# Performance work log

Measured on AMD Instinct MI355X. Metric: run time of the kernel, lower is better.

## Reference

```python
import jax, jax.numpy as jnp
import numpy as np

N_NODES = 200000
N_EDGES = 12800000
N_FEAT = 256


def setup_inputs() -> dict:
    key = jax.random.key(0)
    k1, k2, k3, k4 = jax.random.split(key, 4)
    x = jax.random.normal(k1, (N_NODES, N_FEAT), dtype=jnp.float32)
    edge_index = jax.random.randint(k2, (2, N_EDGES), 0, N_NODES, dtype=jnp.int64)
    attrs = jax.random.uniform(k3, (N_EDGES,), dtype=jnp.float32)
    W = jax.random.normal(k4, (N_FEAT, 1), dtype=jnp.float32) * (1.0 / np.sqrt(N_FEAT))
    b = jnp.zeros((1,), dtype=jnp.float32)
    return {"x": x, "edge_index": edge_index, "attrs": attrs, "W": W, "b": b}


def reference(x, edge_index, attrs, W, b):
    # GCNConv(num_features, 1) with edge_weight=attrs, default add_self_loops=True, normalize=True
    N = x.shape[0]
    row, col = edge_index[0], edge_index[1]  # source, target
    loop = jnp.arange(N, dtype=edge_index.dtype)
    row = jnp.concatenate([row, loop])
    col = jnp.concatenate([col, loop])
    w = jnp.concatenate([attrs, jnp.ones((N,), dtype=x.dtype)])
    # symmetric normalization: deg over targets with edge weights
    deg = jax.ops.segment_sum(w, col, num_segments=N)
    dis = jnp.where(deg > 0, jax.lax.rsqrt(deg), jnp.zeros_like(deg))
    norm = dis[row] * w * dis[col]  # [E+N]
    h = x @ W  # [N, 1]
    msg = norm[:, None] * h[row]  # gather + weight, [E+N, 1]
    out = jax.ops.segment_sum(msg, col, num_segments=N) + b  # scatter-add, [N, 1]
    out = out * jnp.tanh(jax.nn.softplus(out))  # Mish
    return out.reshape(1, -1)
```

## Files before the change

### kernel.cpp

```cpp
#include <hip/hip_runtime.h>
#include <hip/hip_fp16.h>
#include <math.h>
#include <stdint.h>


#define NFEAT 256
#define SPAN 4096
#define SPAN_BITS 12
#define MAXBKT 64
#define SEG 16
#define BCAP 266240
#define TILE 6144
#define PBT 512
#define BBT 512

__global__ void k_zero_u32(unsigned* __restrict__ p, int n) {
    int i = blockIdx.x * blockDim.x + threadIdx.x;
    if (i < n) p[i] = 0u;
}

__global__ void k_matvec(const float* __restrict__ x,
                         const float* __restrict__ W,
                         float* __restrict__ h, int N) {
    int gid  = blockIdx.x * blockDim.x + threadIdx.x;
    int node = gid >> 6;
    int lane = gid & 63;
    if (node >= N) return;
    float4 xv = ((const float4*)(x + (size_t)node * NFEAT))[lane];
    float4 wv = ((const float4*)W)[lane];
    float s = xv.x * wv.x + xv.y * wv.y + xv.z * wv.z + xv.w * wv.w;
#pragma unroll
    for (int off = 32; off > 0; off >>= 1)
        s += __shfl_down(s, off, 64);
    if (lane == 0) h[node] = s;
}

__global__ void __launch_bounds__(PBT) k_partition(
        const int* __restrict__ row, const int* __restrict__ col,
        const float* __restrict__ attrs,
        unsigned* __restrict__ g_cnt,
        unsigned* __restrict__ keys, __half* __restrict__ att16,
        int E, int nbkt) {
    __shared__ unsigned lhist[MAXBKT];
    __shared__ unsigned lstart[MAXBKT];
    __shared__ unsigned lcur[MAXBKT];
    __shared__ unsigned lbase[MAXBKT];
    __shared__ unsigned lkey[TILE];
    __shared__ unsigned short latt[TILE];

    const int tid = threadIdx.x;
    const int e0  = blockIdx.x * TILE;
    const int e1  = min(e0 + TILE, E);
    const int nv  = (e1 - e0) & ~3;

    if (tid < MAXBKT) lhist[tid] = 0u;
    __syncthreads();
    for (int o = tid << 2; o < nv; o += PBT << 2) {
        int4 c4 = *(const int4*)(col + e0 + o);
        atomicAdd(&lhist[((unsigned)c4.x) >> SPAN_BITS], 1u);
        atomicAdd(&lhist[((unsigned)c4.y) >> SPAN_BITS], 1u);
        atomicAdd(&lhist[((unsigned)c4.z) >> SPAN_BITS], 1u);
        atomicAdd(&lhist[((unsigned)c4.w) >> SPAN_BITS], 1u);
    }
    for (int e = e0 + nv + tid; e < e1; e += PBT)
        atomicAdd(&lhist[((unsigned)col[e]) >> SPAN_BITS], 1u);
    __syncthreads();
    if (tid == 0) {
        unsigned s = 0;
        for (int b = 0; b < nbkt; ++b) { lstart[b] = s; s += lhist[b]; }
    }
    if (tid < nbkt) lbase[tid] = atomicAdd(&g_cnt[tid], lhist[tid]);
    __syncthreads();
    if (tid < nbkt) lcur[tid] = lstart[tid];
    __syncthreads();

    for (int o = tid << 2; o < nv; o += PBT << 2) {
        const int e = e0 + o;
        int4   c4 = *(const int4*)(col + e);
        int4   r4 = *(const int4*)(row + e);
        float4 a4 = *(const float4*)(attrs + e);
        {
            unsigned c = (unsigned)c4.x, bkt = c >> SPAN_BITS;
            unsigned t = atomicAdd(&lcur[bkt], 1u);
            lkey[t] = ((unsigned)r4.x << SPAN_BITS) | (c & (SPAN - 1));
            latt[t] = __half_as_ushort(__float2half(a4.x));
        }
        {
            unsigned c = (unsigned)c4.y, bkt = c >> SPAN_BITS;
            unsigned t = atomicAdd(&lcur[bkt], 1u);
            lkey[t] = ((unsigned)r4.y << SPAN_BITS) | (c & (SPAN - 1));
            latt[t] = __half_as_ushort(__float2half(a4.y));
        }
        {
            unsigned c = (unsigned)c4.z, bkt = c >> SPAN_BITS;
            unsigned t = atomicAdd(&lcur[bkt], 1u);
            lkey[t] = ((unsigned)r4.z << SPAN_BITS) | (c & (SPAN - 1));
            latt[t] = __half_as_ushort(__float2half(a4.z));
        }
        {
            unsigned c = (unsigned)c4.w, bkt = c >> SPAN_BITS;
            unsigned t = atomicAdd(&lcur[bkt], 1u);
            lkey[t] = ((unsigned)r4.w << SPAN_BITS) | (c & (SPAN - 1));
            latt[t] = __half_as_ushort(__float2half(a4.w));
        }
    }
    for (int e = e0 + nv + tid; e < e1; e += PBT) {
        unsigned c   = (unsigned)col[e];
        unsigned bkt = c >> SPAN_BITS;
        unsigned t   = atomicAdd(&lcur[bkt], 1u);
        lkey[t] = ((unsigned)row[e] << SPAN_BITS) | (c & (SPAN - 1));
        latt[t] = __half_as_ushort(__float2half(attrs[e]));
    }
    __syncthreads();

    const int wave = tid >> 6, lane = tid & 63;
    for (int b = wave; b < nbkt; b += (PBT / 64)) {
        const unsigned cnt = lhist[b];
        const unsigned gb  = lbase[b];
        const unsigned ls  = lstart[b];
        const size_t base  = (size_t)b * BCAP;
        for (unsigned i = lane; i < cnt; i += 64) {
            unsigned t = gb + i;
            if (t < BCAP) {
                keys[base + t]  = lkey[ls + i];
                att16[base + t] = __ushort_as_half(latt[ls + i]);
            }
        }
    }
}

__global__ void __launch_bounds__(BBT) k_bucket_deg(
        const unsigned* __restrict__ g_cnt, const unsigned* __restrict__ keys,
        const __half* __restrict__ att16, float* __restrict__ rep, int npad) {
    __shared__ float acc[SPAN];
    const int seg = blockIdx.x, bkt = blockIdx.y, tid = threadIdx.x;
#pragma unroll
    for (int j = tid; j < SPAN; j += BBT) acc[j] = 0.f;
    __syncthreads();
    const unsigned cnt = min(g_cnt[bkt], (unsigned)BCAP);
    const unsigned per = (((cnt + SEG - 1) / SEG) + 3u) & ~3u;
    const unsigned i0 = seg * per, i1 = min(cnt, i0 + per);
    const size_t base = (size_t)bkt * BCAP;
    if (i1 > i0) {
        const unsigned count = i1 - i0;
        const unsigned nvec  = count & ~3u;
        const unsigned* kp = keys + base + i0;
        const unsigned short* ap = (const unsigned short*)att16 + base + i0;
        for (unsigned o = tid << 2; o < nvec; o += BBT << 2) {
            uint4   k4 = *(const uint4*)(kp + o);
            ushort4 a4 = *(const ushort4*)(ap + o);
            atomicAdd(&acc[k4.x & (SPAN - 1)], __half2float(__ushort_as_half(a4.x)));
            atomicAdd(&acc[k4.y & (SPAN - 1)], __half2float(__ushort_as_half(a4.y)));
            atomicAdd(&acc[k4.z & (SPAN - 1)], __half2float(__ushort_as_half(a4.z)));
            atomicAdd(&acc[k4.w & (SPAN - 1)], __half2float(__ushort_as_half(a4.w)));
        }
        for (unsigned i = nvec + tid; i < count; i += BBT)
            atomicAdd(&acc[kp[i] & (SPAN - 1)],
                      __half2float(__ushort_as_half(ap[i])));
    }
    __syncthreads();
    float* dst = rep + (size_t)seg * npad + (size_t)bkt * SPAN;
#pragma unroll
    for (int j = tid; j < SPAN; j += BBT) dst[j] = acc[j];
}

__global__ void k_norm(const float* __restrict__ rep,
                       const float* __restrict__ h,
                       float* __restrict__ dis, float* __restrict__ g,
                       int N, int npad) {
    int n = blockIdx.x * blockDim.x + threadIdx.x;
    if (n >= N) return;
    float d = 1.0f;
#pragma unroll
    for (int s = 0; s < SEG; ++s) d += rep[(size_t)s * npad + n];
    float si = rsqrtf(d);
    dis[n] = si;
    g[n]   = si * h[n];
}

__global__ void __launch_bounds__(BBT) k_bucket_scatter(
        const unsigned* __restrict__ g_cnt, const unsigned* __restrict__ keys,
        const __half* __restrict__ att16, const float* __restrict__ g,
        float* __restrict__ rep, int npad) {
    __shared__ float acc[SPAN];
    const int seg = blockIdx.x, bkt = blockIdx.y, tid = threadIdx.x;
#pragma unroll
    for (int j = tid; j < SPAN; j += BBT) acc[j] = 0.f;
    __syncthreads();
    const unsigned cnt = min(g_cnt[bkt], (unsigned)BCAP);
    const unsigned per = (((cnt + SEG - 1) / SEG) + 3u) & ~3u;
    const unsigned i0 = seg * per, i1 = min(cnt, i0 + per);
    const size_t base = (size_t)bkt * BCAP;
    if (i1 > i0) {
        const unsigned count = i1 - i0;
        const unsigned nvec  = count & ~3u;
        const unsigned* kp = keys + base + i0;
        const unsigned short* ap = (const unsigned short*)att16 + base + i0;
        for (unsigned o = tid << 2; o < nvec; o += BBT << 2) {
            uint4   k4 = *(const uint4*)(kp + o);
            ushort4 a4 = *(const ushort4*)(ap + o);
            float m0 = __half2float(__ushort_as_half(a4.x)) * g[k4.x >> SPAN_BITS];
            float m1 = __half2float(__ushort_as_half(a4.y)) * g[k4.y >> SPAN_BITS];
            float m2 = __half2float(__ushort_as_half(a4.z)) * g[k4.z >> SPAN_BITS];
            float m3 = __half2float(__ushort_as_half(a4.w)) * g[k4.w >> SPAN_BITS];
            atomicAdd(&acc[k4.x & (SPAN - 1)], m0);
            atomicAdd(&acc[k4.y & (SPAN - 1)], m1);
            atomicAdd(&acc[k4.z & (SPAN - 1)], m2);
            atomicAdd(&acc[k4.w & (SPAN - 1)], m3);
        }
        for (unsigned i = nvec + tid; i < count; i += BBT) {
            unsigned k = kp[i];
            atomicAdd(&acc[k & (SPAN - 1)],
                      __half2float(__ushort_as_half(ap[i])) * g[k >> SPAN_BITS]);
        }
    }
    __syncthreads();
    float* dst = rep + (size_t)seg * npad + (size_t)bkt * SPAN;
#pragma unroll
    for (int j = tid; j < SPAN; j += BBT) dst[j] = acc[j];
}

__global__ void k_final(const float* __restrict__ rep,
                        const float* __restrict__ dis,
                        const float* __restrict__ g,
                        const float* __restrict__ b,
                        float* __restrict__ out, int N, int npad) {
    int n = blockIdx.x * blockDim.x + threadIdx.x;
    if (n >= N) return;
    float s = 0.f;
#pragma unroll
    for (int k = 0; k < SEG; ++k) s += rep[(size_t)k * npad + n];
    float v  = dis[n] * (s + g[n]) + b[0];
    float sp = (v > 20.0f) ? v : log1pf(expf(v));
    out[n] = v * tanhf(sp);
}

__global__ void f_deg(const int* __restrict__ col, const float* __restrict__ attrs,
                      float* __restrict__ deg, int E) {
    int e = blockIdx.x * blockDim.x + threadIdx.x;
    if (e < E) atomicAdd(deg + col[e], attrs[e]);
}
__global__ void f_init(float* __restrict__ deg, int N) {
    int n = blockIdx.x * blockDim.x + threadIdx.x;
    if (n < N) deg[n] = 1.0f;
}
__global__ void f_norm(float* deg_dis, float* hg, float* __restrict__ acc, int N) {
    int n = blockIdx.x * blockDim.x + threadIdx.x;
    if (n >= N) return;
    float s = rsqrtf(deg_dis[n]);
    float gv = s * hg[n];
    deg_dis[n] = s; hg[n] = gv; acc[n] = s * gv;
}
__global__ void f_scatter(const int* __restrict__ row, const int* __restrict__ col,
                          const float* __restrict__ attrs, const float* __restrict__ g,
                          const float* __restrict__ dis, float* __restrict__ acc, int E) {
    int e = blockIdx.x * blockDim.x + threadIdx.x;
    if (e < E) atomicAdd(acc + col[e], attrs[e] * g[row[e]] * dis[col[e]]);
}
__global__ void f_mish(float* out, const float* __restrict__ b, int N) {
    int n = blockIdx.x * blockDim.x + threadIdx.x;
    if (n >= N) return;
    float v = out[n] + b[0];
    float sp = (v > 20.0f) ? v : log1pf(expf(v));
    out[n] = v * tanhf(sp);
}

extern "C" void kernel_launch(void* const* d_in, const int* in_sizes, int n_in,
                              void* d_out, int out_size, void* d_ws, size_t ws_size,
                              hipStream_t stream) {
    const float* x     = (const float*)d_in[0];
    const int*   ei    = (const int*)d_in[1];
    const float* attrs = (const float*)d_in[2];
    const float* W     = (const float*)d_in[3];
    const float* bias  = (const float*)d_in[4];
    float* out = (float*)d_out;

    const int N = in_sizes[0] / NFEAT;
    const int E = in_sizes[1] / 2;
    const int* row = ei;
    const int* col = ei + E;

    const int nbkt = (N + SPAN - 1) / SPAN;
    const int npad = nbkt * SPAN;

    const size_t need = (size_t)3 * N * 4
                      + (size_t)SEG * npad * 4
                      + (size_t)MAXBKT * 4
                      + (size_t)nbkt * BCAP * 6 + 256;
    const int BT = 256;

    if (ws_size >= need && nbkt <= MAXBKT) {
        float* h   = (float*)d_ws;
        float* dis = h + N;
        float* g   = dis + N;
        float* rep = g + N;
        unsigned* g_cnt = (unsigned*)(rep + (size_t)SEG * npad);
        unsigned* keys  = g_cnt + MAXBKT;
        __half* att16   = (__half*)(keys + (size_t)nbkt * BCAP);

        const int pgrid = (E + TILE - 1) / TILE;

        k_zero_u32<<<1, 64, 0, stream>>>(g_cnt, MAXBKT);
        k_matvec<<<(N + 3) / 4, BT, 0, stream>>>(x, W, h, N);
        k_partition<<<pgrid, PBT, 0, stream>>>(row, col, attrs, g_cnt,
                                               keys, att16, E, nbkt);
        dim3 bg(SEG, nbkt);
        k_bucket_deg<<<bg, BBT, 0, stream>>>(g_cnt, keys, att16, rep, npad);
        k_norm<<<(N + BT - 1) / BT, BT, 0, stream>>>(rep, h, dis, g, N, npad);
        k_bucket_scatter<<<bg, BBT, 0, stream>>>(g_cnt, keys, att16, g, rep, npad);
        k_final<<<(N + BT - 1) / BT, BT, 0, stream>>>(rep, dis, g, bias, out, N, npad);
    } else {
        float* h   = (float*)d_ws;
        float* deg = h + N;
        k_matvec<<<(N + 3) / 4, BT, 0, stream>>>(x, W, h, N);
        f_init<<<(N + BT - 1) / BT, BT, 0, stream>>>(deg, N);
        f_deg<<<(E + BT - 1) / BT, BT, 0, stream>>>(col, attrs, deg, E);
        f_norm<<<(N + BT - 1) / BT, BT, 0, stream>>>(deg, h, out, N);
        f_scatter<<<(E + BT - 1) / BT, BT, 0, stream>>>(row, col, attrs, h, deg, out, E);
        f_mish<<<(N + BT - 1) / BT, BT, 0, stream>>>(out, bias, N);
    }
}
```

Before: 578.1 us.

## Fuse degree accumulation into partition via global atomics, drop bucket_deg pass

Computes node degrees by issuing a global float atomicAdd per edge inside the partition kernel, removing the separate k_bucket_deg pass that re-read all keys and fp16 attrs and wrote SEG-way partial sums. k_norm now reads a single degree array instead of reducing SEG partials. The scatter kernel is also widened to process eight edges per thread with 128-bit loads of keys and packed half attrs. The trade is 12.8M scattered global atomics contending in L2, which may cost more than the removed streaming pass; the degree now uses full-precision attrs rather than fp16.

New measurement: 1.075 ms. 1.86x slower.

```diff
diff --git a/kernel.cpp b/kernel.cpp
--- a/kernel.cpp
+++ b/kernel.cpp
@@ -40,6 +40,7 @@
         const float* __restrict__ attrs,
         unsigned* __restrict__ g_cnt,
         unsigned* __restrict__ keys, __half* __restrict__ att16,
+        float* __restrict__ deg,
         int E, int nbkt) {
     __shared__ unsigned lhist[MAXBKT];
     __shared__ unsigned lstart[MAXBKT];
@@ -84,32 +85,38 @@
             unsigned t = atomicAdd(&lcur[bkt], 1u);
             lkey[t] = ((unsigned)r4.x << SPAN_BITS) | (c & (SPAN - 1));
             latt[t] = __half_as_ushort(__float2half(a4.x));
+            atomicAdd(deg + c, a4.x);
         }
         {
             unsigned c = (unsigned)c4.y, bkt = c >> SPAN_BITS;
             unsigned t = atomicAdd(&lcur[bkt], 1u);
             lkey[t] = ((unsigned)r4.y << SPAN_BITS) | (c & (SPAN - 1));
             latt[t] = __half_as_ushort(__float2half(a4.y));
+            atomicAdd(deg + c, a4.y);
         }
         {
             unsigned c = (unsigned)c4.z, bkt = c >> SPAN_BITS;
             unsigned t = atomicAdd(&lcur[bkt], 1u);
             lkey[t] = ((unsigned)r4.z << SPAN_BITS) | (c & (SPAN - 1));
             latt[t] = __half_as_ushort(__float2half(a4.z));
+            atomicAdd(deg + c, a4.z);
         }
         {
             unsigned c = (unsigned)c4.w, bkt = c >> SPAN_BITS;
             unsigned t = atomicAdd(&lcur[bkt], 1u);
             lkey[t] = ((unsigned)r4.w << SPAN_BITS) | (c & (SPAN - 1));
             latt[t] = __half_as_ushort(__float2half(a4.w));
+            atomicAdd(deg + c, a4.w);
         }
     }
     for (int e = e0 + nv + tid; e < e1; e += PBT) {
         unsigned c   = (unsigned)col[e];
         unsigned bkt = c >> SPAN_BITS;
         unsigned t   = atomicAdd(&lcur[bkt], 1u);
+        float    a   = attrs[e];
         lkey[t] = ((unsigned)row[e] << SPAN_BITS) | (c & (SPAN - 1));
-        latt[t] = __half_as_ushort(__float2half(attrs[e]));
+        latt[t] = __half_as_ushort(__float2half(a));
+        atomicAdd(deg + c, a);
     }
     __syncthreads();
 
@@ -129,50 +136,13 @@
     }
 }
 
-__global__ void __launch_bounds__(BBT) k_bucket_deg(
-        const unsigned* __restrict__ g_cnt, const unsigned* __restrict__ keys,
-        const __half* __restrict__ att16, float* __restrict__ rep, int npad) {
-    __shared__ float acc[SPAN];
-    const int seg = blockIdx.x, bkt = blockIdx.y, tid = threadIdx.x;
-#pragma unroll
-    for (int j = tid; j < SPAN; j += BBT) acc[j] = 0.f;
-    __syncthreads();
-    const unsigned cnt = min(g_cnt[bkt], (unsigned)BCAP);
-    const unsigned per = (((cnt + SEG - 1) / SEG) + 3u) & ~3u;
-    const unsigned i0 = seg * per, i1 = min(cnt, i0 + per);
-    const size_t base = (size_t)bkt * BCAP;
-    if (i1 > i0) {
-        const unsigned count = i1 - i0;
-        const unsigned nvec  = count & ~3u;
-        const unsigned* kp = keys + base + i0;
-        const unsigned short* ap = (const unsigned short*)att16 + base + i0;
-        for (unsigned o = tid << 2; o < nvec; o += BBT << 2) {
-            uint4   k4 = *(const uint4*)(kp + o);
-            ushort4 a4 = *(const ushort4*)(ap + o);
-            atomicAdd(&acc[k4.x & (SPAN - 1)], __half2float(__ushort_as_half(a4.x)));
-            atomicAdd(&acc[k4.y & (SPAN - 1)], __half2float(__ushort_as_half(a4.y)));
-            atomicAdd(&acc[k4.z & (SPAN - 1)], __half2float(__ushort_as_half(a4.z)));
-            atomicAdd(&acc[k4.w & (SPAN - 1)], __half2float(__ushort_as_half(a4.w)));
-        }
-        for (unsigned i = nvec + tid; i < count; i += BBT)
-            atomicAdd(&acc[kp[i] & (SPAN - 1)],
-                      __half2float(__ushort_as_half(ap[i])));
-    }
-    __syncthreads();
-    float* dst = rep + (size_t)seg * npad + (size_t)bkt * SPAN;
-#pragma unroll
-    for (int j = tid; j < SPAN; j += BBT) dst[j] = acc[j];
-}
-
-__global__ void k_norm(const float* __restrict__ rep,
+__global__ void k_norm(const float* __restrict__ deg,
                        const float* __restrict__ h,
                        float* __restrict__ dis, float* __restrict__ g,
-                       int N, int npad) {
+                       int N) {
     int n = blockIdx.x * blockDim.x + threadIdx.x;
     if (n >= N) return;
-    float d = 1.0f;
-#pragma unroll
-    for (int s = 0; s < SEG; ++s) d += rep[(size_t)s * npad + n];
+    float d = 1.0f + deg[n];
     float si = rsqrtf(d);
     dis[n] = si;
     g[n]   = si * h[n];
@@ -188,25 +158,42 @@
     for (int j = tid; j < SPAN; j += BBT) acc[j] = 0.f;
     __syncthreads();
     const unsigned cnt = min(g_cnt[bkt], (unsigned)BCAP);
-    const unsigned per = (((cnt + SEG - 1) / SEG) + 3u) & ~3u;
+    const unsigned per = (((cnt + SEG - 1) / SEG) + 7u) & ~7u;
     const unsigned i0 = seg * per, i1 = min(cnt, i0 + per);
     const size_t base = (size_t)bkt * BCAP;
     if (i1 > i0) {
         const unsigned count = i1 - i0;
-        const unsigned nvec  = count & ~3u;
+        const unsigned nvec  = count & ~7u;
         const unsigned* kp = keys + base + i0;
         const unsigned short* ap = (const unsigned short*)att16 + base + i0;
-        for (unsigned o = tid << 2; o < nvec; o += BBT << 2) {
-            uint4   k4 = *(const uint4*)(kp + o);
-            ushort4 a4 = *(const ushort4*)(ap + o);
-            float m0 = __half2float(__ushort_as_half(a4.x)) * g[k4.x >> SPAN_BITS];
-            float m1 = __half2float(__ushort_as_half(a4.y)) * g[k4.y >> SPAN_BITS];
-            float m2 = __half2float(__ushort_as_half(a4.z)) * g[k4.z >> SPAN_BITS];
-            float m3 = __half2float(__ushort_as_half(a4.w)) * g[k4.w >> SPAN_BITS];
-            atomicAdd(&acc[k4.x & (SPAN - 1)], m0);
-            atomicAdd(&acc[k4.y & (SPAN - 1)], m1);
-            atomicAdd(&acc[k4.z & (SPAN - 1)], m2);
-            atomicAdd(&acc[k4.w & (SPAN - 1)], m3);
+        for (unsigned o = tid << 3; o < nvec; o += BBT << 3) {
+            uint4 ka = *(const uint4*)(kp + o);
+            uint4 kb = *(const uint4*)(kp + o + 4);
+            uint4 av = *(const uint4*)(const void*)(ap + o);
+            float g0 = g[ka.x >> SPAN_BITS];
+            float g1 = g[ka.y >> SPAN_BITS];
+            float g2 = g[ka.z >> SPAN_BITS];
+            float g3 = g[ka.w >> SPAN_BITS];
+            float g4 = g[kb.x >> SPAN_BITS];
+            float g5 = g[kb.y >> SPAN_BITS];
+            float g6 = g[kb.z >> SPAN_BITS];
+            float g7 = g[kb.w >> SPAN_BITS];
+            float a0 = __half2float(__ushort_as_half((unsigned short)(av.x & 0xffffu)));
+            float a1 = __half2float(__ushort_as_half((unsigned short)(av.x >> 16)));
+            float a2 = __half2float(__ushort_as_half((unsigned short)(av.y & 0xffffu)));
+            float a3 = __half2float(__ushort_as_half((unsigned short)(av.y >> 16)));
+            float a4 = __half2float(__ushort_as_half((unsigned short)(av.z & 0xffffu)));
+            float a5 = __half2float(__ushort_as_half((unsigned short)(av.z >> 16)));
+            float a6 = __half2float(__ushort_as_half((unsigned short)(av.w & 0xffffu)));
+            float a7 = __half2float(__ushort_as_half((unsigned short)(av.w >> 16)));
+            atomicAdd(&acc[ka.x & (SPAN - 1)], a0 * g0);
+            atomicAdd(&acc[ka.y & (SPAN - 1)], a1 * g1);
+            atomicAdd(&acc[ka.z & (SPAN - 1)], a2 * g2);
+            atomicAdd(&acc[ka.w & (SPAN - 1)], a3 * g3);
+            atomicAdd(&acc[kb.x & (SPAN - 1)], a4 * g4);
+            atomicAdd(&acc[kb.y & (SPAN - 1)], a5 * g5);
+            atomicAdd(&acc[kb.z & (SPAN - 1)], a6 * g6);
+            atomicAdd(&acc[kb.w & (SPAN - 1)], a7 * g7);
         }
         for (unsigned i = nvec + tid; i < count; i += BBT) {
             unsigned k = kp[i];
@@ -283,9 +270,8 @@
     const int nbkt = (N + SPAN - 1) / SPAN;
     const int npad = nbkt * SPAN;
 
-    const size_t need = (size_t)3 * N * 4
+    const size_t need = (size_t)(4 * N + MAXBKT) * 4
                       + (size_t)SEG * npad * 4
-                      + (size_t)MAXBKT * 4
                       + (size_t)nbkt * BCAP * 6 + 256;
     const int BT = 256;
 
@@ -294,19 +280,20 @@
         float* dis = h + N;
         float* g   = dis + N;
         float* rep = g + N;
-        unsigned* g_cnt = (unsigned*)(rep + (size_t)SEG * npad);
+        float* deg = rep + (size_t)SEG * npad;
+        unsigned* g_cnt = (unsigned*)(deg + N);
         unsigned* keys  = g_cnt + MAXBKT;
         __half* att16   = (__half*)(keys + (size_t)nbkt * BCAP);
 
         const int pgrid = (E + TILE - 1) / TILE;
 
-        k_zero_u32<<<1, 64, 0, stream>>>(g_cnt, MAXBKT);
+        k_zero_u32<<<(N + MAXBKT + BT - 1) / BT, BT, 0, stream>>>(
+            (unsigned*)deg, N + MAXBKT);
         k_matvec<<<(N + 3) / 4, BT, 0, stream>>>(x, W, h, N);
         k_partition<<<pgrid, PBT, 0, stream>>>(row, col, attrs, g_cnt,
-                                               keys, att16, E, nbkt);
+                                               keys, att16, deg, E, nbkt);
+        k_norm<<<(N + BT - 1) / BT, BT, 0, stream>>>(deg, h, dis, g, N);
         dim3 bg(SEG, nbkt);
-        k_bucket_deg<<<bg, BBT, 0, stream>>>(g_cnt, keys, att16, rep, npad);
-        k_norm<<<(N + BT - 1) / BT, BT, 0, stream>>>(rep, h, dis, g, N, npad);
         k_bucket_scatter<<<bg, BBT, 0, stream>>>(g_cnt, keys, att16, g, rep, npad);
         k_final<<<(N + BT - 1) / BT, BT, 0, stream>>>(rep, dis, g, bias, out, N, npad);
     } else {
```
